# Kernel tuning notes

Measured on AMD Instinct MI355X. Metric: run time of the kernel, lower is better.

## Reference

```python
import jax, jax.numpy as jnp
import numpy as np

NGROUP, CIN, COUT, K, HIDDEN = 8, 16, 16, 5, True


def _build_mask():
    # Group-causal PixelCNN-style mask for a 5x5 kernel.
    # Spatial: rows above center fully visible; center row visible left of center.
    # Center tap: input group g_in visible to output group g_out iff
    #   g_in <= g_out (hidden layer) or g_in < g_out (input layer).
    nout, cinall = NGROUP * COUT, NGROUP * CIN
    c = K // 2
    m = np.zeros((nout, cinall, K, K), dtype=np.float32)
    m[:, :, :c, :] = 1.0          # rows strictly above center
    m[:, :, c, :c] = 1.0          # center row, left of center
    g_out = np.arange(nout)[:, None] // COUT   # (nout,1)
    g_in = np.arange(cinall)[None, :] // CIN   # (1,cinall)
    center_ok = (g_in <= g_out) if HIDDEN else (g_in < g_out)
    m[:, :, c, c] = center_ok.astype(np.float32)
    return jnp.asarray(m)

_MASK = _build_mask()


def setup_inputs() -> dict:
    key = jax.random.key(0)
    k1, k2 = jax.random.split(key)
    x = jax.random.normal(k1, (8, 128, 256, 512), dtype=jnp.float32)
    weight = jax.random.uniform(k2, (128, 128, 5, 5), dtype=jnp.float32)
    bias = jnp.zeros((128,), dtype=jnp.float32)
    slope = jnp.zeros((128,), dtype=jnp.float32)  # PReLU slope (zero -> ReLU)
    return {"x": x, "weight": weight, "bias": bias, "slope": slope}


def reference(x, weight, bias, slope):
    w = weight * _MASK  # apply causal group mask
    # context pad by 2 then valid 5x5 conv == SAME padding conv
    y = jax.lax.conv_general_dilated(
        x, w, window_strides=(1, 1), padding=((2, 2), (2, 2)),
        dimension_numbers=("NCHW", "OIHW", "NCHW"))
    y = y + bias[None, :, None, None]
    a = slope[None, :, None, None]
    return jnp.where(y > 0, y, a * y)  # per-channel PReLU
```

## Files before the change

### kernel.cpp

```cpp
#include <hip/hip_runtime.h>
#include <hip/hip_bf16.h>

typedef __attribute__((ext_vector_type(8))) short short8;
typedef __attribute__((ext_vector_type(4))) float f32x4;

#define CH 128
#define H 256
#define W 512
#define PH 258
#define PW 516
#define NTAPS 13
#define P_BYTES (PH * PW * CH * 2)
#define P_SHORTS (PH * PW * CH)
#define KK_SHORTS (PH * PW * 32)
#define CHW (CH * H * W)

#define GRAN_PER_ROW 544
#define NLOADS 52
#define BUF_SHORTS (3328 * 8)
#define ROW_SHORTS (GRAN_PER_ROW * 8)

#define GLD_LDS16(g, l)                                                        \
  __builtin_amdgcn_global_load_lds(                                            \
      (const __attribute__((address_space(1))) void*)(g),                      \
      (__attribute__((address_space(3))) void*)(l), 16, 0, 0)

__global__ void zero_pads(unsigned int* __restrict__ Pd) {
    int row  = blockIdx.x;
    int slab = blockIdx.y;
    unsigned int* base = Pd + (size_t)slab * (P_SHORTS / 2);
    int tid = threadIdx.x;
    if (row < 2) {
#pragma unroll
        for (int kk = 0; kk < 4; ++kk) {
            unsigned int* r = base + (size_t)kk * (KK_SHORTS / 2) +
                              (size_t)row * (PW * 16);
            for (int i = tid; i < PW * 16; i += 256) r[i] = 0u;
        }
    } else {
        int kk  = tid >> 6;
        int seg = (tid >> 4) & 3;
        int col = seg < 2 ? seg : 512 + seg;
        int u   = tid & 15;
        base[(size_t)kk * (KK_SHORTS / 2) + ((size_t)row * PW + col) * 16 + u] = 0u;
    }
}

__global__ void premask_weights(const float* __restrict__ w,
                                __hip_bfloat16* __restrict__ Wt2) {
    int idx  = blockIdx.x * 256 + threadIdx.x;
    int frag = idx >> 9;
    int r    = idx & 511;
    int l    = r >> 3;
    int e    = r & 7;
    int t    = frag >> 5;
    int ob   = (frag >> 2) & 7;
    int kcg  = frag & 3;
    int oc   = ob * 16 + (l & 15);
    int ic   = kcg * 32 + (l >> 4) * 8 + e;
    int ky   = t < 5 ? 0 : (t < 10 ? 1 : 2);
    int kx   = t - ky * 5;
    float v  = w[(oc * CH + ic) * 25 + ky * 5 + kx];
    if (t == 12 && ((ic >> 4) > (oc >> 4))) v = 0.f;
    Wt2[idx] = __float2bfloat16(v);
}

__global__ void transpose_pad_all(const float* __restrict__ x,
                                  __hip_bfloat16* __restrict__ Pbase) {
    __shared__ float tile[32][33];
    const float* xn = x + (size_t)blockIdx.z * CHW;
    unsigned short* P = (unsigned short*)(Pbase + (size_t)blockIdx.z * P_SHORTS);
    int h  = blockIdx.y;
    int wt = blockIdx.x & 15;
    int ct = blockIdx.x >> 4;
    int tx = threadIdx.x & 31;
    int ty = threadIdx.x >> 5;
#pragma unroll
    for (int r = 0; r < 4; ++r) {
        int c = ct * 32 + ty + r * 8;
        tile[ty + r * 8][tx] = xn[(c * H + h) * W + wt * 32 + tx];
    }
    __syncthreads();
    int wl = threadIdx.x >> 3;
    int cq = threadIdx.x & 7;
    union { ushort4 u; __hip_bfloat16 hh[4]; } v;
    v.hh[0] = __float2bfloat16(tile[cq * 4 + 0][wl]);
    v.hh[1] = __float2bfloat16(tile[cq * 4 + 1][wl]);
    v.hh[2] = __float2bfloat16(tile[cq * 4 + 2][wl]);
    v.hh[3] = __float2bfloat16(tile[cq * 4 + 3][wl]);
    *reinterpret_cast<ushort4*>(
        P + (size_t)ct * KK_SHORTS +
        ((size_t)(h + 2) * PW + (wt * 32 + wl + 2)) * 32 + cq * 4) = v.u;
}

__global__ __launch_bounds__(512, 2)
void conv_mfma_all(const __hip_bfloat16* __restrict__ Pbase,
                   const __hip_bfloat16* __restrict__ Wt2,
                   const float* __restrict__ bias,
                   const float* __restrict__ slope,
                   float* __restrict__ out) {
    __shared__ short lds[2 * BUF_SHORTS];
    int d   = blockIdx.x;
    int lid = (d & 7) * 256 + (d >> 3);
    int bz  = lid >> 8;
    int by  = (lid >> 2) & 63;
    int bx  = lid & 3;
    const __hip_bfloat16* P = Pbase + (size_t)bz * P_SHORTS;
    float* outn = out + (size_t)bz * CHW;
    int h0    = by << 2;
    int w0    = bx << 7;
    int tid   = threadIdx.x;
    int lane  = tid & 63;
    int wv    = tid >> 6;
    int l15   = lane & 15;
    int khi   = lane >> 4;
    int ohf   = wv & 1;
    int hp    = (wv >> 1) & 1;
    int pxh   = wv >> 2;

    f32x4 acc[4][2][4];
#pragma unroll
    for (int mi = 0; mi < 4; ++mi)
#pragma unroll
        for (int o = 0; o < 2; ++o)
#pragma unroll
            for (int ni = 0; ni < 4; ++ni)
                acc[mi][o][ni] = (f32x4){0.f, 0.f, 0.f, 0.f};

    const short* Wt2s = (const short*)Wt2;

    int stoff[7];
#pragma unroll
    for (int i = 0; i < 7; ++i) {
        int s    = wv + i * 8;
        int g64  = (s << 6) + lane;
        int row  = (g64 >= 544) + (g64 >= 1088) + (g64 >= 1632) +
                   (g64 >= 2176) + (g64 >= 2720) + (g64 >= 3264);
        int rowc = row < 6 ? row : 5;
        int G    = g64 - row * GRAN_PER_ROW;
        int pair = G >> 3;
        int qd   = (G & 7) ^ (pair & 7);
        int px   = pair * 2 + (qd >> 2);
        int chk  = qd & 3;
        int pxc  = px < 132 ? px : 131;
        stoff[i] = ((h0 + rowc) * PW + (w0 + pxc)) * 32 + chk * 8;
    }
    int bq[5];
#pragma unroll
    for (int kx = 0; kx < 5; ++kx) {
        int pxb  = pxh * 64 + kx + l15;
        int pair = pxb >> 1;
        bq[kx] = ((pair << 3) + ((((pxb & 1) << 2) | khi) ^ (pair & 7))) << 3;
    }

    auto stage = [&](int kk, int bsel) {
        const __hip_bfloat16* Pk = P + (size_t)kk * KK_SHORTS;
#pragma unroll
        for (int i = 0; i < 7; ++i) {
            int s = wv + i * 8;
            if (s < NLOADS)
                GLD_LDS16(Pk + stoff[i],
                          (char*)lds + bsel * (BUF_SHORTS * 2) + (s << 10));
        }
    };

    stage(0, 0);
    __syncthreads();

    for (int kk = 0; kk < 4; ++kk) {
        const int cur = kk & 1;
        if (kk < 3) stage(kk + 1, cur ^ 1);

        const short* apb = Wt2s + ((ohf * 16 + kk) << 9) + (lane << 3);
        const short* bb  = lds + cur * BUF_SHORTS + (hp * 2) * ROW_SHORTS;
#pragma unroll
        for (int kx = 0; kx < 5; ++kx) {
            const int nky = (kx < 3) ? 3 : 2;
            short8 B[4][4];
#pragma unroll
            for (int ni = 0; ni < 4; ++ni) {
                B[0][ni] = *reinterpret_cast<const short8*>(
                    bb + 0 * ROW_SHORTS + bq[kx] + ni * 512);
                B[1][ni] = *reinterpret_cast<const short8*>(
                    bb + 1 * ROW_SHORTS + bq[kx] + ni * 512);
            }
#pragma unroll
            for (int ky = 0; ky < 3; ++ky) {
                if (ky >= nky) break;
                if (ky + 2 <= nky) {
#pragma unroll
                    for (int ni = 0; ni < 4; ++ni)
                        B[ky + 2][ni] = *reinterpret_cast<const short8*>(
                            bb + (ky + 2) * ROW_SHORTS + bq[kx] + ni * 512);
                }
                const short* ap = apb + (ky * 5 + kx) * 16384;
                short8 a[4];
#pragma unroll
                for (int mi = 0; mi < 4; ++mi)
                    a[mi] = *reinterpret_cast<const short8*>(ap + mi * 2048);
                __builtin_amdgcn_s_setprio(1);
#pragma unroll
                for (int mi = 0; mi < 4; ++mi)
#pragma unroll
                    for (int o = 0; o < 2; ++o)
#pragma unroll
                        for (int ni = 0; ni < 4; ++ni)
                            acc[mi][o][ni] = __builtin_amdgcn_mfma_f32_16x16x32_bf16(
                                a[mi], B[ky + o][ni], acc[mi][o][ni], 0, 0, 0);
                __builtin_amdgcn_s_setprio(0);
            }
        }
        __syncthreads();
    }

#pragma unroll
    for (int mi = 0; mi < 4; ++mi) {
        int ocb = ohf * 64 + mi * 16 + 4 * khi;
        f32x4 b4 = *reinterpret_cast<const f32x4*>(bias + ocb);
        f32x4 s4 = *reinterpret_cast<const f32x4*>(slope + ocb);
#pragma unroll
        for (int o = 0; o < 2; ++o) {
            int hrow = h0 + hp * 2 + o;
#pragma unroll
            for (int i = 0; i < 4; ++i) {
                float* orow = outn + ((ocb + i) * H + hrow) * W + w0 + pxh * 64;
#pragma unroll
                for (int ni = 0; ni < 4; ++ni) {
                    float v = acc[mi][o][ni][i] + b4[i];
                    v = v > 0.f ? v : s4[i] * v;
                    orow[ni * 16 + l15] = v;
                }
            }
        }
    }
}

extern "C" void kernel_launch(void* const* d_in, const int* in_sizes, int n_in,
                              void* d_out, int out_size, void* d_ws, size_t ws_size,
                              hipStream_t stream) {
    const float* x      = (const float*)d_in[0];
    const float* weight = (const float*)d_in[1];
    const float* bias   = (const float*)d_in[2];
    const float* slope  = (const float*)d_in[3];
    float* out = (float*)d_out;

    __hip_bfloat16* Pbase = (__hip_bfloat16*)d_ws;
    __hip_bfloat16* Wt2   = (__hip_bfloat16*)((char*)d_ws + 8 * (size_t)P_BYTES);

    zero_pads<<<dim3(PH, 8), 256, 0, stream>>>((unsigned int*)d_ws);
    premask_weights<<<832, 256, 0, stream>>>(weight, Wt2);
    transpose_pad_all<<<dim3(64, 256, 8), 256, 0, stream>>>(x, Pbase);
    conv_mfma_all<<<2048, 512, 0, stream>>>(Pbase, Wt2, bias, slope, out);
}
```

Measured before the change: 554.7 us.

## Interleave next-stage LDS prefetch across kx iterations with per-kx barriers

Splits the global-to-LDS staging of the next channel chunk into pieces issued one or two at a time inside each kx iteration, instead of all at once at the start of the kk loop. It also loads all B rows for a kx up front, adds workgroup barriers around each kx MFMA block, waits on lgkmcnt, and raises priority over the whole block. The goal is to spread memory traffic across the compute and keep waves in lockstep for MFMA issue. The trade-off is extra barrier synchronisation in every kx step and higher register pressure from preloading up to four B rows.

```diff
diff --git a/kernel.cpp b/kernel.cpp
--- a/kernel.cpp
+++ b/kernel.cpp
@@ -153,52 +153,66 @@
         bq[kx] = ((pair << 3) + ((((pxb & 1) << 2) | khi) ^ (pair & 7))) << 3;
     }
 
-    auto stage = [&](int kk, int bsel) {
-        const __hip_bfloat16* Pk = P + (size_t)kk * KK_SHORTS;
-#pragma unroll
-        for (int i = 0; i < 7; ++i) {
-            int s = wv + i * 8;
-            if (s < NLOADS)
-                GLD_LDS16(Pk + stoff[i],
-                          (char*)lds + bsel * (BUF_SHORTS * 2) + (s << 10));
-        }
+    auto stage1 = [&](int kk, int bsel, int i) {
+        int s = wv + i * 8;
+        if (s < NLOADS)
+            GLD_LDS16(P + (size_t)kk * KK_SHORTS + stoff[i],
+                      (char*)lds + bsel * (BUF_SHORTS * 2) + (s << 10));
     };
 
-    stage(0, 0);
+#pragma unroll
+    for (int i = 0; i < 7; ++i) stage1(0, 0, i);
     __syncthreads();
 
     for (int kk = 0; kk < 4; ++kk) {
         const int cur = kk & 1;
-        if (kk < 3) stage(kk + 1, cur ^ 1);
-
         const short* apb = Wt2s + ((ohf * 16 + kk) << 9) + (lane << 3);
         const short* bb  = lds + cur * BUF_SHORTS + (hp * 2) * ROW_SHORTS;
+
 #pragma unroll
         for (int kx = 0; kx < 5; ++kx) {
             const int nky = (kx < 3) ? 3 : 2;
+            if (kk < 3) {
+                if (kx == 0)      { stage1(kk + 1, cur ^ 1, 0);
+                                    stage1(kk + 1, cur ^ 1, 1); }
+                else if (kx == 1) { stage1(kk + 1, cur ^ 1, 2);
+                                    stage1(kk + 1, cur ^ 1, 3); }
+                else              { stage1(kk + 1, cur ^ 1, kx + 2); }
+            }
             short8 B[4][4];
 #pragma unroll
-            for (int ni = 0; ni < 4; ++ni) {
-                B[0][ni] = *reinterpret_cast<const short8*>(
-                    bb + 0 * ROW_SHORTS + bq[kx] + ni * 512);
-                B[1][ni] = *reinterpret_cast<const short8*>(
-                    bb + 1 * ROW_SHORTS + bq[kx] + ni * 512);
-            }
-#pragma unroll
-            for (int ky = 0; ky < 3; ++ky) {
+            for (int r = 0; r < 4; ++r) {
+                if (r > nky) break;
+#pragma unroll
+                for (int ni = 0; ni < 4; ++ni)
+                    B[r][ni] = *reinterpret_cast<const short8*>(
+                        bb + r * ROW_SHORTS + bq[kx] + ni * 512);
+            }
+            short8 a0[4];
+#pragma unroll
+            for (int mi = 0; mi < 4; ++mi)
+                a0[mi] = *reinterpret_cast<const short8*>(
+                    apb + (0 * 5 + kx) * 16384 + mi * 2048);
+            __builtin_amdgcn_s_barrier();
+            asm volatile("s_waitcnt lgkmcnt(0)" ::: "memory");
+            __builtin_amdgcn_sched_barrier(0);
+            __builtin_amdgcn_s_setprio(1);
+#pragma unroll
+            for (int mi = 0; mi < 4; ++mi)
+#pragma unroll
+                for (int o = 0; o < 2; ++o)
+#pragma unroll
+                    for (int ni = 0; ni < 4; ++ni)
+                        acc[mi][o][ni] = __builtin_amdgcn_mfma_f32_16x16x32_bf16(
+                            a0[mi], B[0 + o][ni], acc[mi][o][ni], 0, 0, 0);
+#pragma unroll
+            for (int ky = 1; ky < 3; ++ky) {
                 if (ky >= nky) break;
-                if (ky + 2 <= nky) {
-#pragma unroll
-                    for (int ni = 0; ni < 4; ++ni)
-                        B[ky + 2][ni] = *reinterpret_cast<const short8*>(
-                            bb + (ky + 2) * ROW_SHORTS + bq[kx] + ni * 512);
-                }
-                const short* ap = apb + (ky * 5 + kx) * 16384;
                 short8 a[4];
 #pragma unroll
                 for (int mi = 0; mi < 4; ++mi)
-                    a[mi] = *reinterpret_cast<const short8*>(ap + mi * 2048);
-                __builtin_amdgcn_s_setprio(1);
+                    a[mi] = *reinterpret_cast<const short8*>(
+                        apb + (ky * 5 + kx) * 16384 + mi * 2048);
 #pragma unroll
                 for (int mi = 0; mi < 4; ++mi)
 #pragma unroll
@@ -207,8 +221,9 @@
                         for (int ni = 0; ni < 4; ++ni)
                             acc[mi][o][ni] = __builtin_amdgcn_mfma_f32_16x16x32_bf16(
                                 a[mi], B[ky + o][ni], acc[mi][o][ni], 0, 0, 0);
-                __builtin_amdgcn_s_setprio(0);
-            }
+            }
+            __builtin_amdgcn_s_setprio(0);
+            __builtin_amdgcn_s_barrier();
         }
         __syncthreads();
     }
```

After: 622.1 us. +12.1%, slower.
